# Kernel optimization log

Measured on AMD Instinct MI355X. Metric: run time of the kernel, lower is better.

## Reference

```python
import jax, jax.numpy as jnp
import numpy as np

N = 50000
E = 800000
NFEAT = 128
NHID = 128
NCLASS = 8
BN_EPS = 1e-5
NORM_EPS = 1e-12


def _xavier(key, out_f, in_f):
    lim = float(np.sqrt(6.0 / (in_f + out_f)))
    return jax.random.uniform(key, (out_f, in_f), jnp.float32, -lim, lim)


def setup_inputs() -> dict:
    key = jax.random.key(0)
    ks = jax.random.split(key, 10)
    x = jax.random.normal(ks[0], (N, NFEAT), jnp.float32)
    edge_index = jax.random.randint(ks[1], (2, E), 0, N, jnp.int64)
    return {
        "x": x,
        "edge_index": edge_index,
        # conv1: lin_l (neighbor branch, has bias), lin_r (root branch, no bias)
        "W1l": _xavier(ks[2], NHID, NFEAT),
        "b1l": jnp.zeros((NHID,), jnp.float32),
        "W1r": _xavier(ks[3], NHID, NFEAT),
        # BatchNorm1d(nhid)
        "bn_gamma": jnp.ones((NHID,), jnp.float32),
        "bn_beta": jnp.zeros((NHID,), jnp.float32),
        # conv2
        "W2l": _xavier(ks[4], NHID, NHID),
        "b2l": jnp.zeros((NHID,), jnp.float32),
        "W2r": _xavier(ks[5], NHID, NHID),
        # fc
        "Wfc": _xavier(ks[6], NCLASS, NHID),
        "bfc": jnp.zeros((NCLASS,), jnp.float32),
    }


def _sage_conv(x, src, dst, inv_deg, Wl, bl, Wr):
    # gather neighbor features along edges, scatter-mean into destination nodes
    msg = x[src]                                            # [E, F]
    agg = jax.ops.segment_sum(msg, dst, num_segments=N)      # [N, F]
    agg = agg * inv_deg[:, None]                             # mean aggregation
    out = agg @ Wl.T + bl + x @ Wr.T                         # lin_l(agg) + lin_r(x)
    # L2 normalize per node (normalize=True)
    norm = jnp.sqrt(jnp.sum(out * out, axis=-1, keepdims=True))
    return out / jnp.maximum(norm, NORM_EPS)


def reference(x, edge_index, W1l, b1l, W1r, bn_gamma, bn_beta, W2l, b2l, W2r, Wfc, bfc):
    src, dst = edge_index[0], edge_index[1]
    deg = jax.ops.segment_sum(jnp.ones((E,), x.dtype), dst, num_segments=N)
    inv_deg = jnp.where(deg > 0, 1.0 / jnp.maximum(deg, 1.0), 0.0)

    h = _sage_conv(x, src, dst, inv_deg, W1l, b1l, W1r)

    # transition: ReLU -> BatchNorm1d (batch stats, biased var) -> Dropout (identity, eval)
    h = jax.nn.relu(h)
    mu = jnp.mean(h, axis=0)
    var = jnp.mean((h - mu) ** 2, axis=0)
    h = (h - mu) * jax.lax.rsqrt(var + BN_EPS) * bn_gamma + bn_beta

    h = _sage_conv(h, src, dst, inv_deg, W2l, b2l, W2r)
    return h @ Wfc.T + bfc
```

## Files before the change

### kernel.cpp

```cpp
#include <hip/hip_runtime.h>
#include <hip/hip_bf16.h>

#define NF 128
#define CAP 64

typedef float f4 __attribute__((ext_vector_type(4)));
typedef short s16x8 __attribute__((ext_vector_type(8)));
typedef unsigned short u16x8 __attribute__((ext_vector_type(8)));

static __device__ __forceinline__ unsigned short f2b(float f) {
    union { float f; unsigned u; } c; c.f = f;
    unsigned r = c.u + 0x7fffu + ((c.u >> 16) & 1u);
    return (unsigned short)(r >> 16);
}
static __device__ __forceinline__ float blo(unsigned v) { return __uint_as_float(v << 16); }
static __device__ __forceinline__ float bhi(unsigned v) { return __uint_as_float(v & 0xffff0000u); }

__global__ __launch_bounds__(256) void k_prep(int* __restrict__ zp, int nwords, int ZB,
                                              const float* __restrict__ x,
                                              unsigned* __restrict__ out32, int N,
                                              const float* __restrict__ w0,
                                              const float* __restrict__ w1,
                                              const float* __restrict__ w2,
                                              unsigned short* __restrict__ wt) {
    int b = blockIdx.x;
    if (b < ZB) {
        int i = b * 256 + threadIdx.x;
        if (i < nwords) zp[i] = 0;
    } else if (b < ZB + (N * 64 + 255) / 256) {
        int i = (b - ZB) * 256 + threadIdx.x;
        if (i >= N * 64) return;
        int n = i >> 6, l = i & 63;
        int s = l >> 4, li = l & 15;
        float2 v = *(const float2*)(x + (size_t)n * NF + l * 2);
        out32[(size_t)s * N * 16 + (size_t)n * 16 + li] =
            (unsigned)f2b(v.x) | ((unsigned)f2b(v.y) << 16);
    } else {
        int t = (b - ZB - (N * 64 + 255) / 256) * 256 + threadIdx.x;
        if (t >= 6144) return;
        int mat = t >> 11, rem = t & 2047;
        int col = rem >> 4, ks = (rem >> 2) & 3, qq = rem & 3;
        const float* W = (mat == 0) ? w0 : (mat == 1) ? w1 : w2;
        int layer = (mat == 2) ? 1 : 0, half = (mat == 1) ? 1 : 0;
        const float* src = W + col * NF + ks * 32 + qq * 8;
        u16x8 d;
#pragma unroll
        for (int j = 0; j < 8; ++j) d[j] = f2b(src[j]);
        *(u16x8*)(wt + layer * 65536 + (half * 4 + ks) * 4096 + (col >> 4) * 512 +
                  (qq * 16 + (col & 15)) * 8) = d;
    }
}

__global__ __launch_bounds__(256) void k_fill(const int* __restrict__ ei, int E,
                                              int* __restrict__ cnt,
                                              unsigned short* __restrict__ csr,
                                              int nper) {
    int b = blockIdx.x;
    int i = (b >> 3) * 256 + threadIdx.x;
    if (i >= E) return;
    int d = ei[E + i];
    int lo = (b & 7) * nper;
    if (d >= lo && d < lo + nper) {
        int p = atomicAdd(&cnt[d], 1);
        csr[(size_t)d * CAP + p] = (unsigned short)ei[i];
    }
}

__global__ __launch_bounds__(256) void k_prep_w2(const float* __restrict__ bnSum,
                                                 const float* __restrict__ bnSq,
                                                 const float* __restrict__ gamma,
                                                 const float* __restrict__ beta,
                                                 const float* __restrict__ w2r,
                                                 const float* __restrict__ b2l,
                                                 unsigned short* __restrict__ wtL2,
                                                 float* __restrict__ bias2,
                                                 float* __restrict__ sbn,
                                                 float* __restrict__ bbn, float n) {
    __shared__ float sl[128], bl[128];
    int tid = threadIdx.x;
    if (tid < 128) {
        float su = 0.f, sq = 0.f;
#pragma unroll
        for (int s = 0; s < 8; ++s) { su += bnSum[s * 128 + tid]; sq += bnSq[s * 128 + tid]; }
        float mu = su / n;
        float var = fmaxf(sq / n - mu * mu, 0.f);
        float s = gamma[tid] / sqrtf(var + 1e-5f);
        sl[tid] = s;
        bl[tid] = beta[tid] - mu * s;
    }
    __syncthreads();
    if (blockIdx.x < 8) {
        int t = blockIdx.x * 256 + tid;
        int col = t >> 4, ks = (t >> 2) & 3, qq = t & 3;
        int k0 = ks * 32 + qq * 8;
        u16x8 d;
#pragma unroll
        for (int j = 0; j < 8; ++j) d[j] = f2b(w2r[col * NF + k0 + j] * sl[k0 + j]);
        *(u16x8*)(wtL2 + (4 + ks) * 4096 + (col >> 4) * 512 +
                  (qq * 16 + (col & 15)) * 8) = d;
    } else {
        if (tid < NF) {
            float s = b2l[tid];
            for (int k = 0; k < NF; ++k) s += w2r[tid * NF + k] * bl[k];
            bias2[tid] = s;
            sbn[tid] = sl[tid];
            bbn[tid] = bl[tid];
        }
    }
}

template <bool TR>
__global__ __launch_bounds__(256) void k_agg(const uint4* __restrict__ T4all,
                                             const unsigned short* __restrict__ csr,
                                             const int* __restrict__ deg,
                                             const float* __restrict__ sbn,
                                             const float* __restrict__ bbn,
                                             uint4* __restrict__ outT4, int N) {
    int b = blockIdx.x;
    int s = (b & 7) >> 1;
    int chunk = (b >> 3) * 2 + (b & 1);
    int tid = threadIdx.x;
    int wid = tid >> 6, lane = tid & 63, g = lane >> 4, li = lane & 15;
    int node = chunk * 16 + wid * 4 + g;
    if (node >= N) return;
    int cnt = deg[node];
    int nb = li >> 2, fq = li & 3;
    const uint4* T4 = T4all + (size_t)s * N * 4;
    const unsigned short* cp = csr + (size_t)node * CAP;
    float a0 = 0, a1 = 0, a2 = 0, a3 = 0, a4 = 0, a5 = 0, a6 = 0, a7 = 0;
    int j = 0;
    for (; j + 16 <= cnt; j += 16) {
        int sA = cp[j + nb], sB = cp[j + 4 + nb], sC = cp[j + 8 + nb], sD = cp[j + 12 + nb];
        uint4 vA = T4[(size_t)sA * 4 + fq];
        uint4 vB = T4[(size_t)sB * 4 + fq];
        uint4 vC = T4[(size_t)sC * 4 + fq];
        uint4 vD = T4[(size_t)sD * 4 + fq];
        a0 += (blo(vA.x) + blo(vB.x)) + (blo(vC.x) + blo(vD.x));
        a1 += (bhi(vA.x) + bhi(vB.x)) + (bhi(vC.x) + bhi(vD.x));
        a2 += (blo(vA.y) + blo(vB.y)) + (blo(vC.y) + blo(vD.y));
        a3 += (bhi(vA.y) + bhi(vB.y)) + (bhi(vC.y) + bhi(vD.y));
        a4 += (blo(vA.z) + blo(vB.z)) + (blo(vC.z) + blo(vD.z));
        a5 += (bhi(vA.z) + bhi(vB.z)) + (bhi(vC.z) + bhi(vD.z));
        a6 += (blo(vA.w) + blo(vB.w)) + (blo(vC.w) + blo(vD.w));
        a7 += (bhi(vA.w) + bhi(vB.w)) + (bhi(vC.w) + bhi(vD.w));
    }
    for (; j + 8 <= cnt; j += 8) {
        int sA = cp[j + nb], sB = cp[j + 4 + nb];
        uint4 vA = T4[(size_t)sA * 4 + fq];
        uint4 vB = T4[(size_t)sB * 4 + fq];
        a0 += blo(vA.x) + blo(vB.x); a1 += bhi(vA.x) + bhi(vB.x);
        a2 += blo(vA.y) + blo(vB.y); a3 += bhi(vA.y) + bhi(vB.y);
        a4 += blo(vA.z) + blo(vB.z); a5 += bhi(vA.z) + bhi(vB.z);
        a6 += blo(vA.w) + blo(vB.w); a7 += bhi(vA.w) + bhi(vB.w);
    }
    for (; j < cnt; j += 4) {
        int idx = j + nb;
        bool val = idx < cnt;
        int sA = cp[val ? idx : j];
        uint4 vA = T4[(size_t)sA * 4 + fq];
        if (val) {
            a0 += blo(vA.x); a1 += bhi(vA.x);
            a2 += blo(vA.y); a3 += bhi(vA.y);
            a4 += blo(vA.z); a5 += bhi(vA.z);
            a6 += blo(vA.w); a7 += bhi(vA.w);
        }
    }
    a0 += __shfl_xor(a0, 4); a1 += __shfl_xor(a1, 4);
    a2 += __shfl_xor(a2, 4); a3 += __shfl_xor(a3, 4);
    a4 += __shfl_xor(a4, 4); a5 += __shfl_xor(a5, 4);
    a6 += __shfl_xor(a6, 4); a7 += __shfl_xor(a7, 4);
    a0 += __shfl_xor(a0, 8); a1 += __shfl_xor(a1, 8);
    a2 += __shfl_xor(a2, 8); a3 += __shfl_xor(a3, 8);
    a4 += __shfl_xor(a4, 8); a5 += __shfl_xor(a5, 8);
    a6 += __shfl_xor(a6, 8); a7 += __shfl_xor(a7, 8);
    if (li < 4) {
        float id = (cnt > 0) ? 1.0f / (float)cnt : 0.f;
        float r[8] = {a0 * id, a1 * id, a2 * id, a3 * id,
                      a4 * id, a5 * id, a6 * id, a7 * id};
        if (TR) {
            if (cnt > 0) {
                const float2* sc2 = (const float2*)(sbn + s * 32 + fq * 8);
                const float2* bc2 = (const float2*)(bbn + s * 32 + fq * 8);
#pragma unroll
                for (int i = 0; i < 4; ++i) {
                    float2 sc = sc2[i], bc = bc2[i];
                    r[2 * i]     = r[2 * i]     * sc.x + bc.x;
                    r[2 * i + 1] = r[2 * i + 1] * sc.y + bc.y;
                }
            }
        }
        uint4 p;
        p.x = (unsigned)f2b(r[0]) | ((unsigned)f2b(r[1]) << 16);
        p.y = (unsigned)f2b(r[2]) | ((unsigned)f2b(r[3]) << 16);
        p.z = (unsigned)f2b(r[4]) | ((unsigned)f2b(r[5]) << 16);
        p.w = (unsigned)f2b(r[6]) | ((unsigned)f2b(r[7]) << 16);
        outT4[((size_t)s * N + node) * 4 + fq] = p;
    }
}

template <int MODE>
__global__ __launch_bounds__(256, 2) void k_lin(
    const unsigned short* __restrict__ aggB,
    const unsigned short* __restrict__ src2,
    const unsigned short* __restrict__ wt,
    const float* __restrict__ bias,
    const float* __restrict__ wfc, const float* __restrict__ bfc,
    unsigned short* __restrict__ outb,
    float* __restrict__ outf,
    float* __restrict__ bnSum, float* __restrict__ bnSq, int N) {
    __shared__ __align__(16) unsigned short wlds[32768];
    __shared__ float sbuf[1024];

    int tid = threadIdx.x;
    int lane = tid & 63;
    int q = lane >> 4, m = lane & 15;
    int wv = tid >> 6;

    s16x8 afr[2][8];
#pragma unroll
    for (int t = 0; t < 2; ++t) {
        int rb = blockIdx.x * 128 + t * 64 + wv * 16;
        int r = rb + m; if (r >= N) r = N - 1;
        size_t rr = (size_t)r * 32 + q * 8;
#pragma unroll
        for (int ks = 0; ks < 4; ++ks)
            afr[t][ks] = *(const s16x8*)(aggB + (size_t)ks * N * 32 + rr);
#pragma unroll
        for (int ks = 0; ks < 4; ++ks)
            afr[t][4 + ks] = *(const s16x8*)(src2 + (size_t)ks * N * 32 + rr);
    }
    {
        const f4* wsrc4 = (const f4*)wt;
        f4* wd4 = (f4*)wlds;
#pragma unroll
        for (int it = 0; it < 16; ++it) wd4[tid + it * 256] = wsrc4[tid + it * 256];
    }
    if constexpr (MODE == 1) {
        if (tid < 256) sbuf[tid] = 0.f;
    } else {
        *(f4*)&sbuf[tid * 4] = ((const f4*)wfc)[tid];
    }
    __syncthreads();

    const unsigned short* wb = wlds + lane * 8;

#pragma unroll
    for (int t = 0; t < 2; ++t) {
        int row_base = blockIdx.x * 128 + t * 64 + wv * 16;
        f4 acc[8];
#pragma unroll
        for (int c = 0; c < 8; ++c) acc[c] = (f4){0.f, 0.f, 0.f, 0.f};
#pragma unroll
        for (int ks = 0; ks < 8; ++ks) {
#pragma unroll
            for (int c = 0; c < 8; ++c) {
                s16x8 bfr = *(const s16x8*)(wb + ks * 4096 + c * 512);
                acc[c] = __builtin_amdgcn_mfma_f32_16x16x32_bf16(afr[t][ks], bfr, acc[c], 0, 0, 0);
            }
        }
#pragma unroll
        for (int c = 0; c < 8; ++c) {
            float b = bias[c * 16 + m];
#pragma unroll
            for (int i = 0; i < 4; ++i) acc[c][i] += b;
        }
        float ss[4];
#pragma unroll
        for (int i = 0; i < 4; ++i) {
            float s = 0.f;
#pragma unroll
            for (int c = 0; c < 8; ++c) s += acc[c][i] * acc[c][i];
            s += __shfl_xor(s, 1); s += __shfl_xor(s, 2);
            s += __shfl_xor(s, 4); s += __shfl_xor(s, 8);
            ss[i] = 1.0f / fmaxf(sqrtf(s), 1e-12f);
        }
#pragma unroll
        for (int c = 0; c < 8; ++c)
#pragma unroll
            for (int i = 0; i < 4; ++i) acc[c][i] *= ss[i];

        if constexpr (MODE == 1) {
#pragma unroll
            for (int c = 0; c < 8; ++c)
#pragma unroll
                for (int i = 0; i < 4; ++i) acc[c][i] = fmaxf(acc[c][i], 0.f);
#pragma unroll
            for (int i = 0; i < 4; ++i) {
                int row = row_base + q * 4 + i;
                if (row < N) {
#pragma unroll
                    for (int c = 0; c < 8; ++c)
                        outb[(size_t)(c >> 1) * N * 32 + (size_t)row * 32 + (c & 1) * 16 + m] =
                            f2b(acc[c][i]);
                }
            }
            float su[8], sq[8];
#pragma unroll
            for (int c = 0; c < 8; ++c) { su[c] = 0.f; sq[c] = 0.f; }
#pragma unroll
            for (int i = 0; i < 4; ++i) {
                bool vi = (row_base + q * 4 + i) < N;
#pragma unroll
                for (int c = 0; c < 8; ++c) {
                    float u = vi ? acc[c][i] : 0.f;
                    su[c] += u; sq[c] += u * u;
                }
            }
#pragma unroll
            for (int c = 0; c < 8; ++c) {
                su[c] += __shfl_xor(su[c], 16); su[c] += __shfl_xor(su[c], 32);
                sq[c] += __shfl_xor(sq[c], 16); sq[c] += __shfl_xor(sq[c], 32);
            }
            if (lane < 16) {
#pragma unroll
                for (int c = 0; c < 8; ++c) {
                    atomicAdd(&sbuf[c * 16 + m], su[c]);
                    atomicAdd(&sbuf[128 + c * 16 + m], sq[c]);
                }
            }
        } else {
            float o[8][4];
#pragma unroll
            for (int cls = 0; cls < 8; ++cls)
#pragma unroll
                for (int i = 0; i < 4; ++i) o[cls][i] = 0.f;
#pragma unroll
            for (int cls = 0; cls < 8; ++cls) {
#pragma unroll
                for (int c = 0; c < 8; ++c) {
                    float wv2 = sbuf[cls * NF + c * 16 + m];
#pragma unroll
                    for (int i = 0; i < 4; ++i) o[cls][i] += acc[c][i] * wv2;
                }
#pragma unroll
                for (int i = 0; i < 4; ++i) {
                    float tt = o[cls][i];
                    tt += __shfl_xor(tt, 1); tt += __shfl_xor(tt, 2);
                    tt += __shfl_xor(tt, 4); tt += __shfl_xor(tt, 8);
                    o[cls][i] = tt;
                }
            }
            float sel[4] = {0.f, 0.f, 0.f, 0.f};
#pragma unroll
            for (int cls = 0; cls < 8; ++cls) {
                bool p = (m == cls);
#pragma unroll
                for (int i = 0; i < 4; ++i) sel[i] = p ? o[cls][i] : sel[i];
            }
            if (m < 8) {
                float bb = bfc[m];
#pragma unroll
                for (int i = 0; i < 4; ++i) {
                    int row = row_base + q * 4 + i;
                    if (row < N) outf[(size_t)row * 8 + m] = sel[i] + bb;
                }
            }
        }
    }

    if constexpr (MODE == 1) {
        __syncthreads();
        int shard = (blockIdx.x & 7) * 128;
        if (tid < 128)      atomicAdd(&bnSum[shard + tid], sbuf[tid]);
        else if (tid < 256) atomicAdd(&bnSq[shard + tid - 128], sbuf[tid]);
    }
}

extern "C" void kernel_launch(void* const* d_in, const int* in_sizes, int n_in,
                              void* d_out, int out_size, void* d_ws, size_t ws_size,
                              hipStream_t stream) {
    const float* x   = (const float*)d_in[0];
    const int*   ei  = (const int*)d_in[1];
    const float* W1l = (const float*)d_in[2];
    const float* b1l = (const float*)d_in[3];
    const float* W1r = (const float*)d_in[4];
    const float* gam = (const float*)d_in[5];
    const float* bet = (const float*)d_in[6];
    const float* W2l = (const float*)d_in[7];
    const float* b2l = (const float*)d_in[8];
    const float* W2r = (const float*)d_in[9];
    const float* Wfc = (const float*)d_in[10];
    const float* bfc = (const float*)d_in[11];
    int N = in_sizes[0] / NF;
    int E = in_sizes[1] / 2;

    char* w = (char*)d_ws;
    size_t o = 0;
#define ALO(nbytes) (o = (o + 255) & ~(size_t)255, o += (nbytes), (w + o - (nbytes)))
    int* cnt    = (int*)ALO((size_t)N * 4);
    float* bnSum = (float*)ALO(4096);
    float* bnSq  = (float*)ALO(4096);
    size_t zwords = o / 4;
    unsigned short* csr = (unsigned short*)ALO((size_t)N * CAP * 2);
    unsigned short* wt  = (unsigned short*)ALO((size_t)2 * 65536 * 2);
    float* sbn   = (float*)ALO(512);
    float* bbn   = (float*)ALO(512);
    float* bias2 = (float*)ALO(512);
    unsigned short* xb   = (unsigned short*)ALO((size_t)N * NF * 2);
    unsigned short* aggB = (unsigned short*)ALO((size_t)N * NF * 2);
    unsigned short* h1b  = (unsigned short*)ALO((size_t)N * NF * 2);
#undef ALO
    (void)ws_size; (void)n_in; (void)out_size;

    int EB8 = ((E + 255) / 256) * 8;
    int nper = (N + 7) / 8;
    int aggBlocks = ((N + 31) / 32) * 8;
    int LB2 = (N + 127) / 128;
    int CV = (N * 64 + 255) / 256;
    int ZB = (int)((zwords + 255) / 256);

    k_prep<<<ZB + CV + 24, 256, 0, stream>>>((int*)d_ws, (int)zwords, ZB,
                                             x, (unsigned*)xb, N, W1l, W1r, W2l, wt);
    k_fill<<<EB8, 256, 0, stream>>>(ei, E, cnt, csr, nper);

    k_agg<false><<<aggBlocks, 256, 0, stream>>>((const uint4*)xb, csr, cnt,
                                                nullptr, nullptr, (uint4*)aggB, N);
    k_lin<1><<<LB2, 256, 0, stream>>>(aggB, xb, wt, b1l, nullptr, nullptr,
                                      h1b, nullptr, bnSum, bnSq, N);
    k_prep_w2<<<9, 256, 0, stream>>>(bnSum, bnSq, gam, bet, W2r, b2l,
                                     wt + 65536, bias2, sbn, bbn, (float)N);
    k_agg<true><<<aggBlocks, 256, 0, stream>>>((const uint4*)h1b, csr, cnt,
                                               sbn, bbn, (uint4*)aggB, N);
    k_lin<2><<<LB2, 256, 0, stream>>>(aggB, h1b, wt + 65536, bias2, Wfc, bfc,
                                      nullptr, (float*)d_out, nullptr, nullptr, N);
}
```

Measured before the change: 156.5 us.

## Pad CSR with a zero sentinel row to remove aggregation tail loops

Adds an extra all-zero node row (index N) to each bf16 feature buffer and pre-fills the CSR neighbor table with that sentinel index. The aggregation kernel then rounds each degree up to a multiple of 16 and runs only the 16-wide unrolled loop, dropping the 8-wide and masked remainder loops and their divergence. The cost is extra gathers of the zero row (cached) for padded slots, plus a full CSR initialization pass (N*64 shorts) in the prep kernel. The linear kernel is changed to write a zero row at index N and every buffer stride becomes N+1.

```diff
diff --git a/kernel.cpp b/kernel.cpp
--- a/kernel.cpp
+++ b/kernel.cpp
@@ -17,6 +17,8 @@
 static __device__ __forceinline__ float bhi(unsigned v) { return __uint_as_float(v & 0xffff0000u); }
 
 __global__ __launch_bounds__(256) void k_prep(int* __restrict__ zp, int nwords, int ZB,
+                                              int SB,
+                                              unsigned* __restrict__ csr32, int csrWords,
                                               const float* __restrict__ x,
                                               unsigned* __restrict__ out32, int N,
                                               const float* __restrict__ w0,
@@ -24,19 +26,28 @@
                                               const float* __restrict__ w2,
                                               unsigned short* __restrict__ wt) {
     int b = blockIdx.x;
+    int S = N + 1;
+    int CV2 = (S * 64 + 255) / 256;
     if (b < ZB) {
         int i = b * 256 + threadIdx.x;
         if (i < nwords) zp[i] = 0;
-    } else if (b < ZB + (N * 64 + 255) / 256) {
+    } else if (b < ZB + SB) {
         int i = (b - ZB) * 256 + threadIdx.x;
-        if (i >= N * 64) return;
+        unsigned sv = ((unsigned)N << 16) | (unsigned)N;
+        if (i < csrWords) csr32[i] = sv;
+    } else if (b < ZB + SB + CV2) {
+        int i = (b - ZB - SB) * 256 + threadIdx.x;
+        if (i >= S * 64) return;
         int n = i >> 6, l = i & 63;
         int s = l >> 4, li = l & 15;
-        float2 v = *(const float2*)(x + (size_t)n * NF + l * 2);
-        out32[(size_t)s * N * 16 + (size_t)n * 16 + li] =
-            (unsigned)f2b(v.x) | ((unsigned)f2b(v.y) << 16);
+        unsigned pv = 0;
+        if (n < N) {
+            float2 v = *(const float2*)(x + (size_t)n * NF + l * 2);
+            pv = (unsigned)f2b(v.x) | ((unsigned)f2b(v.y) << 16);
+        }
+        out32[(size_t)s * S * 16 + (size_t)n * 16 + li] = pv;
     } else {
-        int t = (b - ZB - (N * 64 + 255) / 256) * 256 + threadIdx.x;
+        int t = (b - ZB - SB - CV2) * 256 + threadIdx.x;
         if (t >= 6144) return;
         int mat = t >> 11, rem = t & 2047;
         int col = rem >> 4, ks = (rem >> 2) & 3, qq = rem & 3;
@@ -117,6 +128,7 @@
                                              const float* __restrict__ bbn,
                                              uint4* __restrict__ outT4, int N) {
     int b = blockIdx.x;
+    int S = N + 1;
     int s = (b & 7) >> 1;
     int chunk = (b >> 3) * 2 + (b & 1);
     int tid = threadIdx.x;
@@ -124,12 +136,12 @@
     int node = chunk * 16 + wid * 4 + g;
     if (node >= N) return;
     int cnt = deg[node];
+    int cntR = (cnt + 15) & ~15;
     int nb = li >> 2, fq = li & 3;
-    const uint4* T4 = T4all + (size_t)s * N * 4;
+    const uint4* T4 = T4all + (size_t)s * S * 4;
     const unsigned short* cp = csr + (size_t)node * CAP;
     float a0 = 0, a1 = 0, a2 = 0, a3 = 0, a4 = 0, a5 = 0, a6 = 0, a7 = 0;
-    int j = 0;
-    for (; j + 16 <= cnt; j += 16) {
+    for (int j = 0; j < cntR; j += 16) {
         int sA = cp[j + nb], sB = cp[j + 4 + nb], sC = cp[j + 8 + nb], sD = cp[j + 12 + nb];
         uint4 vA = T4[(size_t)sA * 4 + fq];
         uint4 vB = T4[(size_t)sB * 4 + fq];
@@ -143,27 +155,6 @@
         a5 += (bhi(vA.z) + bhi(vB.z)) + (bhi(vC.z) + bhi(vD.z));
         a6 += (blo(vA.w) + blo(vB.w)) + (blo(vC.w) + blo(vD.w));
         a7 += (bhi(vA.w) + bhi(vB.w)) + (bhi(vC.w) + bhi(vD.w));
-    }
-    for (; j + 8 <= cnt; j += 8) {
-        int sA = cp[j + nb], sB = cp[j + 4 + nb];
-        uint4 vA = T4[(size_t)sA * 4 + fq];
-        uint4 vB = T4[(size_t)sB * 4 + fq];
-        a0 += blo(vA.x) + blo(vB.x); a1 += bhi(vA.x) + bhi(vB.x);
-        a2 += blo(vA.y) + blo(vB.y); a3 += bhi(vA.y) + bhi(vB.y);
-        a4 += blo(vA.z) + blo(vB.z); a5 += bhi(vA.z) + bhi(vB.z);
-        a6 += blo(vA.w) + blo(vB.w); a7 += bhi(vA.w) + bhi(vB.w);
-    }
-    for (; j < cnt; j += 4) {
-        int idx = j + nb;
-        bool val = idx < cnt;
-        int sA = cp[val ? idx : j];
-        uint4 vA = T4[(size_t)sA * 4 + fq];
-        if (val) {
-            a0 += blo(vA.x); a1 += bhi(vA.x);
-            a2 += blo(vA.y); a3 += bhi(vA.y);
-            a4 += blo(vA.z); a5 += bhi(vA.z);
-            a6 += blo(vA.w); a7 += bhi(vA.w);
-        }
     }
     a0 += __shfl_xor(a0, 4); a1 += __shfl_xor(a1, 4);
     a2 += __shfl_xor(a2, 4); a3 += __shfl_xor(a3, 4);
@@ -194,7 +185,7 @@
         p.y = (unsigned)f2b(r[2]) | ((unsigned)f2b(r[3]) << 16);
         p.z = (unsigned)f2b(r[4]) | ((unsigned)f2b(r[5]) << 16);
         p.w = (unsigned)f2b(r[6]) | ((unsigned)f2b(r[7]) << 16);
-        outT4[((size_t)s * N + node) * 4 + fq] = p;
+        outT4[((size_t)s * S + node) * 4 + fq] = p;
     }
 }
 
@@ -212,6 +203,7 @@
     __shared__ float sbuf[1024];
 
     int tid = threadIdx.x;
+    int S = N + 1;
     int lane = tid & 63;
     int q = lane >> 4, m = lane & 15;
     int wv = tid >> 6;
@@ -224,10 +216,10 @@
         size_t rr = (size_t)r * 32 + q * 8;
 #pragma unroll
         for (int ks = 0; ks < 4; ++ks)
-            afr[t][ks] = *(const s16x8*)(aggB + (size_t)ks * N * 32 + rr);
+            afr[t][ks] = *(const s16x8*)(aggB + (size_t)ks * S * 32 + rr);
 #pragma unroll
         for (int ks = 0; ks < 4; ++ks)
-            afr[t][4 + ks] = *(const s16x8*)(src2 + (size_t)ks * N * 32 + rr);
+            afr[t][4 + ks] = *(const s16x8*)(src2 + (size_t)ks * S * 32 + rr);
     }
     {
         const f4* wsrc4 = (const f4*)wt;
@@ -287,11 +279,11 @@
 #pragma unroll
             for (int i = 0; i < 4; ++i) {
                 int row = row_base + q * 4 + i;
-                if (row < N) {
+                if (row <= N) {
 #pragma unroll
                     for (int c = 0; c < 8; ++c)
-                        outb[(size_t)(c >> 1) * N * 32 + (size_t)row * 32 + (c & 1) * 16 + m] =
-                            f2b(acc[c][i]);
+                        outb[(size_t)(c >> 1) * S * 32 + (size_t)row * 32 + (c & 1) * 16 + m] =
+                            (row < N) ? f2b(acc[c][i]) : (unsigned short)0;
                 }
             }
             float su[8], sq[8];
@@ -383,6 +375,7 @@
     const float* bfc = (const float*)d_in[11];
     int N = in_sizes[0] / NF;
     int E = in_sizes[1] / 2;
+    int S = N + 1;
 
     char* w = (char*)d_ws;
     size_t o = 0;
@@ -396,9 +389,9 @@
     float* sbn   = (float*)ALO(512);
     float* bbn   = (float*)ALO(512);
     float* bias2 = (float*)ALO(512);
-    unsigned short* xb   = (unsigned short*)ALO((size_t)N * NF * 2);
-    unsigned short* aggB = (unsigned short*)ALO((size_t)N * NF * 2);
-    unsigned short* h1b  = (unsigned short*)ALO((size_t)N * NF * 2);
+    unsigned short* xb   = (unsigned short*)ALO((size_t)S * NF * 2);
+    unsigned short* aggB = (unsigned short*)ALO((size_t)S * NF * 2);
+    unsigned short* h1b  = (unsigned short*)ALO((size_t)S * NF * 2);
 #undef ALO
     (void)ws_size; (void)n_in; (void)out_size;
 
@@ -406,11 +399,14 @@
     int nper = (N + 7) / 8;
     int aggBlocks = ((N + 31) / 32) * 8;
     int LB2 = (N + 127) / 128;
-    int CV = (N * 64 + 255) / 256;
+    int CV2 = (S * 64 + 255) / 256;
     int ZB = (int)((zwords + 255) / 256);
-
-    k_prep<<<ZB + CV + 24, 256, 0, stream>>>((int*)d_ws, (int)zwords, ZB,
-                                             x, (unsigned*)xb, N, W1l, W1r, W2l, wt);
+    int csrWords = N * CAP / 2;
+    int SB = (csrWords + 255) / 256;
+
+    k_prep<<<ZB + SB + CV2 + 24, 256, 0, stream>>>((int*)d_ws, (int)zwords, ZB, SB,
+                                                   (unsigned*)csr, csrWords,
+                                                   x, (unsigned*)xb, N, W1l, W1r, W2l, wt);
     k_fill<<<EB8, 256, 0, stream>>>(ei, E, cnt, csr, nper);
 
     k_agg<false><<<aggBlocks, 256, 0, stream>>>((const uint4*)xb, csr, cnt,
```

Result: faster. 152.5 us (median of 2 runs) (-2.5%).
